# Performance work log

Measured on AMD Instinct MI355X. Metric: run time of the kernel, lower is better.

## Reference

```python
import jax, jax.numpy as jnp
import numpy as np

INPUT_DIM = 512
OUTPUT_DIM = 2048
GAMMA = 0.5
N_ROWS = 65536


def setup_inputs() -> dict:
    key = jax.random.key(0)
    kx, kw, kb = jax.random.split(key, 3)
    input_tensor = jax.random.normal(kx, (N_ROWS, INPUT_DIM), dtype=jnp.float32)
    # RBFSampler.fit: random_weights_ = sqrt(2*gamma) * N(0,1), random_offset_ ~ U(0, 2pi)
    W = jnp.sqrt(2.0 * GAMMA) * jax.random.normal(kw, (INPUT_DIM, OUTPUT_DIM), dtype=jnp.float32)
    b = jax.random.uniform(kb, (OUTPUT_DIM,), dtype=jnp.float32, minval=0.0, maxval=2.0 * np.pi)
    return {"input_tensor": input_tensor, "W": W, "b": b}


def reference(input_tensor, W, b):
    # RBFSampler.transform: cos(X @ W + b) * sqrt(2 / n_components)
    proj = input_tensor @ W + b  # [N, output_dim]
    scale = jnp.sqrt(jnp.asarray(2.0 / OUTPUT_DIM, dtype=proj.dtype))
    return jnp.cos(proj) * scale
```

## Files before the change

kernel.cpp:

```cpp
#include <hip/hip_runtime.h>

typedef __bf16 bf16x8 __attribute__((ext_vector_type(8)));
typedef float  f32x4  __attribute__((ext_vector_type(4)));
typedef int    i32x4  __attribute__((ext_vector_type(4)));
typedef char   c16    __attribute__((ext_vector_type(16)));

constexpr int M_ROWS = 65536;
constexpr int N_COLS = 2048;
constexpr int K_DIM  = 512;
constexpr int NKQ    = 8;
constexpr int MBQ    = 512;
constexpr int NBQ    = 16;

constexpr size_t AQ_OFF  = (65536 + 2048) * 4;
constexpr size_t AQ_SZ   = (size_t)MBQ * NKQ * 16384;
constexpr size_t WQ_OFF  = AQ_OFF + AQ_SZ;
constexpr size_t WQ_SZ   = (size_t)NBQ * NKQ * 16384;
constexpr size_t NEEDQ   = WQ_OFF + WQ_SZ;

__device__ __forceinline__ unsigned short f2bf(float f){
  unsigned int u = __float_as_uint(f);
  u += 0x7FFFu + ((u >> 16) & 1u);
  return (unsigned short)(u >> 16);
}
__device__ __forceinline__ float bf2f(unsigned short h){
  return __uint_as_float(((unsigned int)h) << 16);
}
__device__ __forceinline__ void split4(const float4& v, ushort4& h, ushort4& l){
  h.x = f2bf(v.x); l.x = f2bf(v.x - bf2f(h.x));
  h.y = f2bf(v.y); l.y = f2bf(v.y - bf2f(h.y));
  h.z = f2bf(v.z); l.z = f2bf(v.z - bf2f(h.z));
  h.w = f2bf(v.w); l.w = f2bf(v.w - bf2f(h.w));
}

__device__ __forceinline__ void gl_lds16(const void* g, void* l){
  __builtin_amdgcn_global_load_lds(
      (const __attribute__((address_space(1))) unsigned int*)g,
      (__attribute__((address_space(3))) unsigned int*)l, 16, 0, 0);
}

constexpr float INV2PI = 0.15915494309189535f;
__device__ __forceinline__ float cos_scaled(float v){
  float rev = v * INV2PI;
  rev -= floorf(rev);
  return 0.03125f * __builtin_amdgcn_cosf(rev);
}

__device__ __forceinline__ void q2(float x, float inv, char& o1, char& o2){
  float t1 = x * inv;
  float r1 = rintf(t1);
  float r2 = fminf(rintf((t1 - r1) * 256.0f), 127.0f);
  o1 = (char)(int)r1;
  o2 = (char)(int)r2;
}

__global__ void pack_xq(const float* __restrict__ X, char* __restrict__ AQ,
                        float* __restrict__ sXo){
  const int bid = blockIdx.x;
  const int t = threadIdx.x;
  const int rl = t >> 3, seg = t & 7;
  const int grow = bid * 32 + rl;
  const float* src = X + (size_t)grow * K_DIM + seg * 64;
  f32x4 v[16];
  #pragma unroll
  for (int i = 0; i < 16; ++i)
    v[i] = __builtin_nontemporal_load(reinterpret_cast<const f32x4*>(src) + i);
  float m = 0.f;
  #pragma unroll
  for (int i = 0; i < 16; ++i)
    m = fmaxf(m, fmaxf(fmaxf(fabsf(v[i].x), fabsf(v[i].y)),
                       fmaxf(fabsf(v[i].z), fabsf(v[i].w))));
  m = fmaxf(m, __shfl_xor(m, 1));
  m = fmaxf(m, __shfl_xor(m, 2));
  m = fmaxf(m, __shfl_xor(m, 4));
  m = fmaxf(m, 1e-10f);
  if (seg == 0) sXo[grow] = m * (1.0f / 127.0f);
  const float inv = 127.0f / m;

  const int mb = bid >> 2;
  const int rowt = (bid & 3) * 32 + rl;
  const int i_ = rowt >> 4, r_ = rowt & 15;
  char* tb = AQ + (size_t)(mb * NKQ + seg) * 16384;
  #pragma unroll
  for (int q = 0; q < 4; ++q){
    c16 o1, o2;
    #pragma unroll
    for (int u = 0; u < 4; ++u){
      f32x4 xv = v[q * 4 + u];
      #pragma unroll
      for (int w = 0; w < 4; ++w){
        char a, b; q2(xv[w], inv, a, b);
        o1[u * 4 + w] = a; o2[u * 4 + w] = b;
      }
    }
    int c = i_ * 64 + q * 16 + r_;
    *reinterpret_cast<c16*>(tb + c * 16)        = o1;
    *reinterpret_cast<c16*>(tb + 8192 + c * 16) = o2;
  }
}

__global__ void scale_w(const float* __restrict__ W, float* __restrict__ sWo){
  __shared__ float red[8][32];
  int t = threadIdx.x, nl = t & 31, kq = t >> 5;
  int n = blockIdx.x * 32 + nl;
  float m = 0.f;
  for (int k = kq * 64; k < kq * 64 + 64; ++k)
    m = fmaxf(m, fabsf(W[(size_t)k * N_COLS + n]));
  red[kq][nl] = m;
  __syncthreads();
  if (kq == 0){
    #pragma unroll
    for (int u = 1; u < 8; ++u) m = fmaxf(m, red[u][nl]);
    sWo[n] = fmaxf(m, 1e-10f) * (1.0f / 127.0f);
  }
}

__global__ void pack_wq(const float* __restrict__ W, const float* __restrict__ sW,
                        char* __restrict__ WQ){
  __shared__ float tf[64][132];
  const int nb = blockIdx.x, kt = blockIdx.y, t = threadIdx.x;
  const int kr = t >> 2, nq = t & 3;
  #pragma unroll
  for (int it = 0; it < 8; ++it){
    f32x4 v4 = *reinterpret_cast<const f32x4*>(
        W + (size_t)(kt * 64 + kr) * N_COLS + nb * 128 + nq * 32 + it * 4);
    *reinterpret_cast<f32x4*>(&tf[kr][nq * 32 + it * 4]) = v4;
  }
  __syncthreads();
  char* tb = WQ + (size_t)(nb * NKQ + kt) * 16384;
  #pragma unroll
  for (int cc = 0; cc < 2; ++cc){
    int c = t + cc * 256;
    int jj = c >> 6, q = (c >> 4) & 3, fc = c & 15;
    int col_local = (jj >> 2) * 64 + fc * 4 + (jj & 3);
    float inv = 1.0f / sW[nb * 128 + col_local];
    c16 o1, o2;
    #pragma unroll
    for (int e = 0; e < 16; ++e){
      char a, b; q2(tf[q * 16 + e][col_local], inv, a, b);
      o1[e] = a; o2[e] = b;
    }
    *reinterpret_cast<c16*>(tb + c * 16)        = o1;
    *reinterpret_cast<c16*>(tb + 8192 + c * 16) = o2;
  }
}

#define MFMAI(a,b,c) __builtin_amdgcn_mfma_i32_16x16x64_i8(a,b,c,0,0,0)
#define DRAIN_BAR() { asm volatile("s_waitcnt vmcnt(0)" ::: "memory"); \
                      __builtin_amdgcn_sched_barrier(0); __syncthreads(); }

__launch_bounds__(256, 2)
__global__ void rbf_gemm_i8(const char* __restrict__ AQ, const char* __restrict__ WQ,
                            const float* __restrict__ sX, const float* __restrict__ sW,
                            const float* __restrict__ bvec, float* __restrict__ out){
  __shared__ __align__(16) char smem[2 * 32768];

  int orig = blockIdx.x;
  int wgid = (orig & 7) * 1024 + (orig >> 3);
  int mb = wgid >> 4, nb = wgid & 15;
  int m0 = mb * 128, n0 = nb * 128;

  int tid = threadIdx.x, lane = tid & 63, wid = tid >> 6;
  int wm = wid >> 1, wn = wid & 1;
  int r = lane & 15, g = lane >> 4;

  const char* abase = AQ + (size_t)mb * NKQ * 16384;
  const char* bbase = WQ + (size_t)nb * NKQ * 16384;
  const int bsoff = wid * 1024 + lane * 16;
  const int bdoff = wid * 1024;

  int aoffs[4], boffs[4];
  #pragma unroll
  for (int i = 0; i < 4; ++i) aoffs[i] = (wm * 4 + i) * 1024 + lane * 16;
  #pragma unroll
  for (int j = 0; j < 4; ++j) boffs[j] = (wn * 4 + j) * 1024 + lane * 16;

  i32x4 accm[4][4], accc[4][4];
  #pragma unroll
  for (int i = 0; i < 4; ++i)
    #pragma unroll
    for (int j = 0; j < 4; ++j){
      accm[i][j] = (i32x4){0,0,0,0};
      accc[i][j] = (i32x4){0,0,0,0};
    }

  #pragma unroll
  for (int it = 0; it < 8; ++it)
    gl_lds16(bbase + it * 4096 + bsoff, smem + it * 4096 + bdoff);
  DRAIN_BAR();

  #pragma unroll 1
  for (int t = 0; t < 4; ++t){
    const char* SB = smem + (t & 1) * 32768;

    i32x4 a1[2][4], a2[2][4];
    #pragma unroll
    for (int kq = 0; kq < 2; ++kq){
      const char* ab = abase + (size_t)(2 * t + kq) * 16384;
      #pragma unroll
      for (int i = 0; i < 4; ++i){
        a1[kq][i] = *reinterpret_cast<const i32x4*>(ab + aoffs[i]);
        a2[kq][i] = *reinterpret_cast<const i32x4*>(ab + 8192 + aoffs[i]);
      }
    }

    if (t < 3){
      const char* s = bbase + (size_t)(t + 1) * 32768;
      char* d = smem + ((t + 1) & 1) * 32768;
      #pragma unroll
      for (int it = 0; it < 8; ++it)
        gl_lds16(s + it * 4096 + bsoff, d + it * 4096 + bdoff);
    }

    #pragma unroll
    for (int kq = 0; kq < 2; ++kq){
      const char* SBk = SB + kq * 16384;
      #pragma unroll
      for (int j = 0; j < 4; ++j){
        i32x4 b1 = *reinterpret_cast<const i32x4*>(SBk + boffs[j]);
        i32x4 b2 = *reinterpret_cast<const i32x4*>(SBk + 8192 + boffs[j]);
        #pragma unroll
        for (int i = 0; i < 4; ++i){
          accm[i][j] = MFMAI(a1[kq][i], b1, accm[i][j]);
          accc[i][j] = MFMAI(a1[kq][i], b2, accc[i][j]);
          accc[i][j] = MFMAI(a2[kq][i], b1, accc[i][j]);
        }
      }
    }

    DRAIN_BAR();
  }

  int colb = n0 + wn * 64 + r * 4;
  f32x4 sw4 = *reinterpret_cast<const f32x4*>(sW + colb);
  f32x4 bv  = *reinterpret_cast<const f32x4*>(bvec + colb);
  #pragma unroll
  for (int i = 0; i < 4; ++i){
    int rowb = m0 + wm * 64 + i * 16 + g * 4;
    f32x4 sx4 = *reinterpret_cast<const f32x4*>(sX + rowb);
    #pragma unroll
    for (int p = 0; p < 4; ++p){
      float sx = sx4[p];
      f32x4 o;
      o.x = cos_scaled(fmaf(sx * sw4.x,
              (float)accm[i][0][p] + (float)accc[i][0][p] * 0.00390625f, bv.x));
      o.y = cos_scaled(fmaf(sx * sw4.y,
              (float)accm[i][1][p] + (float)accc[i][1][p] * 0.00390625f, bv.y));
      o.z = cos_scaled(fmaf(sx * sw4.z,
              (float)accm[i][2][p] + (float)accc[i][2][p] * 0.00390625f, bv.z));
      o.w = cos_scaled(fmaf(sx * sw4.w,
              (float)accm[i][3][p] + (float)accc[i][3][p] * 0.00390625f, bv.w));
      __builtin_nontemporal_store(o,
          reinterpret_cast<f32x4*>(out + (size_t)(rowb + p) * N_COLS + colb));
    }
  }
}

#define MFMA_(a,b,c) __builtin_amdgcn_mfma_f32_16x16x32_bf16(a,b,c,0,0,0)
constexpr int LDSK = 40;
constexpr int SEC  = 128 * LDSK;
__launch_bounds__(256, 2)
__global__ void rbf_gemm_nows(const float* __restrict__ X, const float* __restrict__ W,
                              const float* __restrict__ bvec, float* __restrict__ out){
  __shared__ __align__(16) unsigned short smem[4 * SEC];
  int orig = blockIdx.x;
  int wgid = (orig & 7) * (int)(gridDim.x >> 3) + (orig >> 3);
  int mb = wgid >> 4, nb = wgid & 15;
  int m0 = mb * 128, n0 = nb * 128;
  int tid = threadIdx.x, lane = tid & 63, wid = tid >> 6;
  int wm = wid >> 1, wn = wid & 1;
  int r = lane & 15, g = lane >> 4;

  const float* asrc[4]; int alofs[4]; float4 ra[4];
  const float* wsrc[4]; int wnq4[4]; int wkr[4]; float4 rw[4];
  #pragma unroll
  for (int i = 0; i < 4; ++i){
    int c = tid + i * 256;
    int row = c >> 3, q = c & 7;
    asrc[i]  = X + (size_t)(m0 + row) * K_DIM + q * 4;
    alofs[i] = row * LDSK + q * 4;
  }
  #pragma unroll
  for (int i = 0; i < 4; ++i) ra[i] = *reinterpret_cast<const float4*>(asrc[i]);
  #pragma unroll
  for (int i = 0; i < 4; ++i){
    int c = tid + i * 256;
    int kr = c >> 5, nq = c & 31;
    wsrc[i] = W + (size_t)kr * N_COLS + n0 + nq * 4;
    wkr[i] = kr; wnq4[i] = nq * 4;
  }
  #pragma unroll
  for (int i = 0; i < 4; ++i) rw[i] = *reinterpret_cast<const float4*>(wsrc[i]);

  f32x4 acc[4][4];
  #pragma unroll
  for (int i = 0; i < 4; ++i)
    #pragma unroll
    for (int j = 0; j < 4; ++j) acc[i][j] = (f32x4){0.f,0.f,0.f,0.f};

  int aoff[4], boff[4];
  #pragma unroll
  for (int i = 0; i < 4; ++i) aoff[i] = (wm*64 + i*16 + r) * LDSK + g * 8;
  #pragma unroll
  for (int j = 0; j < 4; ++j) boff[j] = (wn*64 + j*16 + r) * LDSK + g * 8;

  #pragma unroll 1
  for (int kt = 0; kt < 16; ++kt){
    __syncthreads();
    #pragma unroll
    for (int i = 0; i < 4; ++i){
      ushort4 h, l;
      split4(ra[i], h, l);
      *reinterpret_cast<ushort4*>(&smem[alofs[i]])       = h;
      *reinterpret_cast<ushort4*>(&smem[SEC + alofs[i]]) = l;
    }
    #pragma unroll
    for (int i = 0; i < 4; ++i){
      float vv[4] = {rw[i].x, rw[i].y, rw[i].z, rw[i].w};
      #pragma unroll
      for (int w2 = 0; w2 < 4; ++w2){
        unsigned short h = f2bf(vv[w2]);
        unsigned short l = f2bf(vv[w2] - bf2f(h));
        int n = wnq4[i] + w2;
        smem[2*SEC + n*LDSK + wkr[i]] = h;
        smem[3*SEC + n*LDSK + wkr[i]] = l;
      }
    }
    if (kt < 15){
      #pragma unroll
      for (int i = 0; i < 4; ++i)
        ra[i] = *reinterpret_cast<const float4*>(asrc[i] + (kt+1)*32);
      #pragma unroll
      for (int i = 0; i < 4; ++i)
        rw[i] = *reinterpret_cast<const float4*>(wsrc[i] + (size_t)(kt+1)*32*N_COLS);
    }
    __syncthreads();
    bf16x8 ah[4], al[4], bh[4], bl[4];
    #pragma unroll
    for (int i = 0; i < 4; ++i){
      ah[i] = *reinterpret_cast<const bf16x8*>(&smem[aoff[i]]);
      al[i] = *reinterpret_cast<const bf16x8*>(&smem[SEC + aoff[i]]);
    }
    #pragma unroll
    for (int j = 0; j < 4; ++j){
      bh[j] = *reinterpret_cast<const bf16x8*>(&smem[2*SEC + boff[j]]);
      bl[j] = *reinterpret_cast<const bf16x8*>(&smem[3*SEC + boff[j]]);
    }
    #pragma unroll
    for (int i = 0; i < 4; ++i){
      #pragma unroll
      for (int j = 0; j < 4; ++j){
        acc[i][j] = MFMA_(ah[i], bh[j], acc[i][j]);
        acc[i][j] = MFMA_(al[i], bh[j], acc[i][j]);
        acc[i][j] = MFMA_(ah[i], bl[j], acc[i][j]);
      }
    }
  }

  float bvv[4];
  #pragma unroll
  for (int j = 0; j < 4; ++j) bvv[j] = bvec[n0 + wn*64 + j*16 + r];
  #pragma unroll
  for (int i = 0; i < 4; ++i){
    #pragma unroll
    for (int j = 0; j < 4; ++j){
      int col = n0 + wn*64 + j*16 + r;
      #pragma unroll
      for (int p = 0; p < 4; ++p){
        int row = m0 + wm*64 + i*16 + g*4 + p;
        out[(size_t)row * N_COLS + col] = cos_scaled(acc[i][j][p] + bvv[j]);
      }
    }
  }
}

extern "C" void kernel_launch(void* const* d_in, const int* in_sizes, int n_in,
                              void* d_out, int out_size, void* d_ws, size_t ws_size,
                              hipStream_t stream){
  const float* X = (const float*)d_in[0];
  const float* W = (const float*)d_in[1];
  const float* b = (const float*)d_in[2];
  float* out = (float*)d_out;
  char* ws = (char*)d_ws;

  if (ws && ws_size >= NEEDQ){
    float* sX = (float*)ws;
    float* sW = (float*)(ws + 65536 * 4);
    char*  AQ = ws + AQ_OFF;
    char*  WQ = ws + WQ_OFF;
    pack_xq<<<2048, 256, 0, stream>>>(X, AQ, sX);
    scale_w<<<64, 256, 0, stream>>>(W, sW);
    pack_wq<<<dim3(NBQ, NKQ), 256, 0, stream>>>(W, sW, WQ);
    rbf_gemm_i8<<<8192, 256, 0, stream>>>(AQ, WQ, sX, sW, b, out);
  } else {
    rbf_gemm_nows<<<8192, 256, 0, stream>>>(X, W, b, out);
  }
}
```

Measured before the change: 320.9 us.

## Make int8 GEMM persistent with full W panel resident in LDS

The int8 GEMM now launches 512 workgroups of 512 threads. Each one loads its whole 128-column quantized W panel (128 KB) into LDS once, then loops over 16 row blocks, streaming A fragments from global memory and writing the cosine epilogue for each block. This removes repeated W staging and the per-iteration barriers and double buffering. In exchange there is only one workgroup per CU, no overlap between A loads and the epilogue, and a smaller per-wave tile.

```diff
diff --git a/kernel.cpp b/kernel.cpp
--- a/kernel.cpp
+++ b/kernel.cpp
@@ -146,112 +146,99 @@
 }
 
 #define MFMAI(a,b,c) __builtin_amdgcn_mfma_i32_16x16x64_i8(a,b,c,0,0,0)
-#define DRAIN_BAR() { asm volatile("s_waitcnt vmcnt(0)" ::: "memory"); \
-                      __builtin_amdgcn_sched_barrier(0); __syncthreads(); }
-
-__launch_bounds__(256, 2)
+
+__launch_bounds__(512, 1)
 __global__ void rbf_gemm_i8(const char* __restrict__ AQ, const char* __restrict__ WQ,
                             const float* __restrict__ sX, const float* __restrict__ sW,
                             const float* __restrict__ bvec, float* __restrict__ out){
-  __shared__ __align__(16) char smem[2 * 32768];
+  __shared__ __align__(16) char smem[131072];
 
   int orig = blockIdx.x;
-  int wgid = (orig & 7) * 1024 + (orig >> 3);
-  int mb = wgid >> 4, nb = wgid & 15;
-  int m0 = mb * 128, n0 = nb * 128;
+  int wgid = (orig & 7) * 64 + (orig >> 3);
+  int mbg = wgid >> 4, nb = wgid & 15;
+  int n0 = nb * 128;
 
   int tid = threadIdx.x, lane = tid & 63, wid = tid >> 6;
   int wm = wid >> 1, wn = wid & 1;
   int r = lane & 15, g = lane >> 4;
 
-  const char* abase = AQ + (size_t)mb * NKQ * 16384;
   const char* bbase = WQ + (size_t)nb * NKQ * 16384;
-  const int bsoff = wid * 1024 + lane * 16;
-  const int bdoff = wid * 1024;
-
-  int aoffs[4], boffs[4];
-  #pragma unroll
-  for (int i = 0; i < 4; ++i) aoffs[i] = (wm * 4 + i) * 1024 + lane * 16;
+  const int soff = wid * 1024 + lane * 16;
+  const int doff = wid * 1024;
+
+  #pragma unroll
+  for (int it = 0; it < 16; ++it)
+    gl_lds16(bbase + it * 8192 + soff, smem + it * 8192 + doff);
+  asm volatile("s_waitcnt vmcnt(0)" ::: "memory");
+  __builtin_amdgcn_sched_barrier(0);
+  __syncthreads();
+
+  int aoffs[2], boffs[4];
+  #pragma unroll
+  for (int i = 0; i < 2; ++i) aoffs[i] = (wm * 2 + i) * 1024 + lane * 16;
   #pragma unroll
   for (int j = 0; j < 4; ++j) boffs[j] = (wn * 4 + j) * 1024 + lane * 16;
 
-  i32x4 accm[4][4], accc[4][4];
-  #pragma unroll
-  for (int i = 0; i < 4; ++i)
-    #pragma unroll
-    for (int j = 0; j < 4; ++j){
-      accm[i][j] = (i32x4){0,0,0,0};
-      accc[i][j] = (i32x4){0,0,0,0};
-    }
-
-  #pragma unroll
-  for (int it = 0; it < 8; ++it)
-    gl_lds16(bbase + it * 4096 + bsoff, smem + it * 4096 + bdoff);
-  DRAIN_BAR();
+  int colb = n0 + wn * 64 + r * 4;
+  f32x4 sw4 = *reinterpret_cast<const f32x4*>(sW + colb);
+  f32x4 bv  = *reinterpret_cast<const f32x4*>(bvec + colb);
 
   #pragma unroll 1
-  for (int t = 0; t < 4; ++t){
-    const char* SB = smem + (t & 1) * 32768;
-
-    i32x4 a1[2][4], a2[2][4];
-    #pragma unroll
-    for (int kq = 0; kq < 2; ++kq){
-      const char* ab = abase + (size_t)(2 * t + kq) * 16384;
-      #pragma unroll
-      for (int i = 0; i < 4; ++i){
-        a1[kq][i] = *reinterpret_cast<const i32x4*>(ab + aoffs[i]);
-        a2[kq][i] = *reinterpret_cast<const i32x4*>(ab + 8192 + aoffs[i]);
-      }
-    }
-
-    if (t < 3){
-      const char* s = bbase + (size_t)(t + 1) * 32768;
-      char* d = smem + ((t + 1) & 1) * 32768;
-      #pragma unroll
-      for (int it = 0; it < 8; ++it)
-        gl_lds16(s + it * 4096 + bsoff, d + it * 4096 + bdoff);
-    }
-
-    #pragma unroll
-    for (int kq = 0; kq < 2; ++kq){
-      const char* SBk = SB + kq * 16384;
+  for (int t = 0; t < 16; ++t){
+    const int mb = mbg * 16 + t;
+    const char* abase = AQ + (size_t)mb * NKQ * 16384;
+
+    i32x4 accm[2][4], accc[2][4];
+    #pragma unroll
+    for (int i = 0; i < 2; ++i)
+      #pragma unroll
+      for (int j = 0; j < 4; ++j){
+        accm[i][j] = (i32x4){0,0,0,0};
+        accc[i][j] = (i32x4){0,0,0,0};
+      }
+
+    #pragma unroll
+    for (int kt = 0; kt < NKQ; ++kt){
+      const char* ab = abase + (size_t)kt * 16384;
+      i32x4 a1[2], a2[2];
+      #pragma unroll
+      for (int i = 0; i < 2; ++i){
+        a1[i] = *reinterpret_cast<const i32x4*>(ab + aoffs[i]);
+        a2[i] = *reinterpret_cast<const i32x4*>(ab + 8192 + aoffs[i]);
+      }
+      const char* SBk = smem + kt * 16384;
       #pragma unroll
       for (int j = 0; j < 4; ++j){
         i32x4 b1 = *reinterpret_cast<const i32x4*>(SBk + boffs[j]);
         i32x4 b2 = *reinterpret_cast<const i32x4*>(SBk + 8192 + boffs[j]);
         #pragma unroll
-        for (int i = 0; i < 4; ++i){
-          accm[i][j] = MFMAI(a1[kq][i], b1, accm[i][j]);
-          accc[i][j] = MFMAI(a1[kq][i], b2, accc[i][j]);
-          accc[i][j] = MFMAI(a2[kq][i], b1, accc[i][j]);
+        for (int i = 0; i < 2; ++i){
+          accm[i][j] = MFMAI(a1[i], b1, accm[i][j]);
+          accc[i][j] = MFMAI(a1[i], b2, accc[i][j]);
+          accc[i][j] = MFMAI(a2[i], b1, accc[i][j]);
         }
       }
     }
 
-    DRAIN_BAR();
-  }
-
-  int colb = n0 + wn * 64 + r * 4;
-  f32x4 sw4 = *reinterpret_cast<const f32x4*>(sW + colb);
-  f32x4 bv  = *reinterpret_cast<const f32x4*>(bvec + colb);
-  #pragma unroll
-  for (int i = 0; i < 4; ++i){
-    int rowb = m0 + wm * 64 + i * 16 + g * 4;
-    f32x4 sx4 = *reinterpret_cast<const f32x4*>(sX + rowb);
-    #pragma unroll
-    for (int p = 0; p < 4; ++p){
-      float sx = sx4[p];
-      f32x4 o;
-      o.x = cos_scaled(fmaf(sx * sw4.x,
-              (float)accm[i][0][p] + (float)accc[i][0][p] * 0.00390625f, bv.x));
-      o.y = cos_scaled(fmaf(sx * sw4.y,
-              (float)accm[i][1][p] + (float)accc[i][1][p] * 0.00390625f, bv.y));
-      o.z = cos_scaled(fmaf(sx * sw4.z,
-              (float)accm[i][2][p] + (float)accc[i][2][p] * 0.00390625f, bv.z));
-      o.w = cos_scaled(fmaf(sx * sw4.w,
-              (float)accm[i][3][p] + (float)accc[i][3][p] * 0.00390625f, bv.w));
-      __builtin_nontemporal_store(o,
-          reinterpret_cast<f32x4*>(out + (size_t)(rowb + p) * N_COLS + colb));
+    #pragma unroll
+    for (int i = 0; i < 2; ++i){
+      int rowb = mb * 128 + wm * 32 + i * 16 + g * 4;
+      f32x4 sx4 = *reinterpret_cast<const f32x4*>(sX + rowb);
+      #pragma unroll
+      for (int p = 0; p < 4; ++p){
+        float sx = sx4[p];
+        f32x4 o;
+        o.x = cos_scaled(fmaf(sx * sw4.x,
+                (float)accm[i][0][p] + (float)accc[i][0][p] * 0.00390625f, bv.x));
+        o.y = cos_scaled(fmaf(sx * sw4.y,
+                (float)accm[i][1][p] + (float)accc[i][1][p] * 0.00390625f, bv.y));
+        o.z = cos_scaled(fmaf(sx * sw4.z,
+                (float)accm[i][2][p] + (float)accc[i][2][p] * 0.00390625f, bv.z));
+        o.w = cos_scaled(fmaf(sx * sw4.w,
+                (float)accm[i][3][p] + (float)accc[i][3][p] * 0.00390625f, bv.w));
+        __builtin_nontemporal_store(o,
+            reinterpret_cast<f32x4*>(out + (size_t)(rowb + p) * N_COLS + colb));
+      }
     }
   }
 }
@@ -391,7 +378,7 @@
     pack_xq<<<2048, 256, 0, stream>>>(X, AQ, sX);
     scale_w<<<64, 256, 0, stream>>>(W, sW);
     pack_wq<<<dim3(NBQ, NKQ), 256, 0, stream>>>(W, sW, WQ);
-    rbf_gemm_i8<<<8192, 256, 0, stream>>>(AQ, WQ, sX, sW, b, out);
+    rbf_gemm_i8<<<512, 512, 0, stream>>>(AQ, WQ, sX, sW, b, out);
   } else {
     rbf_gemm_nows<<<8192, 256, 0, stream>>>(X, W, b, out);
   }
```

New measurement: 609.7 us. 90.0% more time.
